# Performance work log

Measured on AMD Instinct MI355X. Metric: run time of the kernel, lower is better.

Reference implementation:

```python
import jax, jax.numpy as jnp
import numpy as np

NUM_GRAPHS = 512
NODES_PER_GRAPH = 128
HIDDEN = 64
K = 24


def _param(key, shape, scale=0.05):
    return jax.random.normal(key, shape, dtype=jnp.float32) * scale


def setup_inputs() -> dict:
    key = jax.random.key(0)
    ks = jax.random.split(key, 24)
    N = NUM_GRAPHS * NODES_PER_GRAPH
    inp = {
        "x_pf": jax.random.normal(ks[0], (N, 4), dtype=jnp.float32),
        "batch_pf": jnp.repeat(jnp.arange(NUM_GRAPHS, dtype=jnp.int64), NODES_PER_GRAPH),
        # pf_encode: Linear(4,64), ELU, Linear(64,64), ELU
        "we1": _param(ks[1], (4, HIDDEN)), "be1": _param(ks[2], (HIDDEN,)),
        "we2": _param(ks[3], (HIDDEN, HIDDEN)), "be2": _param(ks[4], (HIDDEN,)),
        # three DynamicEdgeConv edge MLPs: Linear(128,64)+ELU
        "wc1": _param(ks[5], (2 * HIDDEN, HIDDEN)), "bc1": _param(ks[6], (HIDDEN,)),
        "wc2": _param(ks[7], (2 * HIDDEN, HIDDEN)), "bc2": _param(ks[8], (HIDDEN,)),
        "wc3": _param(ks[9], (2 * HIDDEN, HIDDEN)), "bc3": _param(ks[10], (HIDDEN,)),
        # output MLP 64->64->32->32->8->1
        "wo1": _param(ks[11], (HIDDEN, 64)), "bo1": _param(ks[12], (64,)),
        "wo2": _param(ks[13], (64, 32)), "bo2": _param(ks[14], (32,)),
        "wo3": _param(ks[15], (32, 32)), "bo3": _param(ks[16], (32,)),
        "wo4": _param(ks[17], (32, 8)), "bo4": _param(ks[18], (8,)),
        "wo5": _param(ks[19], (8, 1)), "bo5": _param(ks[20], (1,)),
    }
    return inp


def dynamic_edge_conv(x, wc, bc):
    """x: [G,P,D]. kNN (incl. self) in feature space per graph, edge feature
    [x_i, x_j - x_i] -> Linear+ELU -> max over neighbors. Matches PyG
    DynamicEdgeConv(nn, k, aggr='max')."""
    sq = jnp.sum(x * x, axis=-1)                                   # [G,P]
    d = sq[:, :, None] + sq[:, None, :] - 2.0 * jnp.einsum('gpd,gqd->gpq', x, x)
    _, idx = jax.lax.top_k(-d, K)                                   # [G,P,K] nearest (self included, dist 0)
    xj = jax.vmap(lambda xg, ig: xg[ig])(x, idx)                    # [G,P,K,D]
    xi = x[:, :, None, :]
    e = jnp.concatenate([jnp.broadcast_to(xi, xj.shape), xj - xi], axis=-1)  # [G,P,K,2D]
    h = jax.nn.elu(e @ wc + bc)                                     # [G,P,K,D]
    return jnp.max(h, axis=2)                                       # [G,P,D]


def reference(x_pf, batch_pf, we1, be1, we2, be2, wc1, bc1, wc2, bc2, wc3, bc3,
              wo1, bo1, wo2, bo2, wo3, bo3, wo4, bo4, wo5, bo5):
    elu = jax.nn.elu
    h = elu(elu(x_pf @ we1 + be1) @ we2 + be2)                      # [N,64]
    h = h.reshape(NUM_GRAPHS, NODES_PER_GRAPH, HIDDEN)              # equal-size graphs
    h = dynamic_edge_conv(h, wc1, bc1)
    h = dynamic_edge_conv(h, wc2, bc2)
    h = dynamic_edge_conv(h, wc3, bc3)
    pooled = jnp.sum(h, axis=1)                                     # global_add_pool -> [G,64]
    o = elu(pooled @ wo1 + bo1)
    o = elu(o @ wo2 + bo2)
    o = elu(o @ wo3 + bo3)
    o = elu(o @ wo4 + bo4)
    out = o @ wo5 + bo5                                             # [G,1]
    return (out, batch_pf)
```

## Files before the change

kernel.cpp:

```cpp
#include <hip/hip_runtime.h>
#include <math.h>

#define NG 512
#define NP 128
#define HID 64
#define KNN 24
#define NTOT (NG*NP)

typedef __attribute__((ext_vector_type(8)))  short  short8;
typedef __attribute__((ext_vector_type(16))) float  floatx16;

__device__ __forceinline__ float elu_f(float v) { return v > 0.0f ? v : expm1f(v); }

__device__ __forceinline__ void split_bf16(float x, unsigned short& hb, unsigned short& lb) {
    unsigned u = __float_as_uint(x);
    unsigned h = (u + 0x7FFFu + ((u >> 16) & 1u)) >> 16;
    hb = (unsigned short)h;
    float hf = __uint_as_float(h << 16);
    float lo = x - hf;
    unsigned v = __float_as_uint(lo);
    lb = (unsigned short)((v + 0x7FFFu + ((v >> 16) & 1u)) >> 16);
}
__device__ __forceinline__ unsigned short bf_rne(float x) {
    unsigned u = __float_as_uint(x);
    return (unsigned short)((u + 0x7FFFu + ((u >> 16) & 1u)) >> 16);
}
__device__ __forceinline__ float bf_lo(unsigned u) { return __uint_as_float(u << 16); }
__device__ __forceinline__ float bf_hi(unsigned u) { return __uint_as_float(u & 0xFFFF0000u); }

__device__ __forceinline__ unsigned short* hchunk(unsigned short* base, int row, int ch) {
    return base + (((row << 4) + (ch ^ (row & 15))) << 3);
}
__device__ __forceinline__ const unsigned short* hchunk(const unsigned short* base, int row, int ch) {
    return base + (((row << 4) + (ch ^ (row & 15))) << 3);
}

__device__ __forceinline__ void sort8_asc(unsigned* y) {
    #pragma unroll
    for (int k = 2; k <= 8; k <<= 1)
        #pragma unroll
        for (int j = k >> 1; j > 0; j >>= 1)
            #pragma unroll
            for (int i = 0; i < 8; ++i) {
                const int l = i ^ j;
                if (l > i) {
                    const bool up = ((i & k) == 0);
                    const unsigned a = y[i], b = y[l];
                    const unsigned mn = a < b ? a : b;
                    const unsigned mx = a < b ? b : a;
                    y[i] = up ? mn : mx;
                    y[l] = up ? mx : mn;
                }
            }
}

__device__ __forceinline__ void merge_top24(unsigned* x) {
    #pragma unroll
    for (int d = 16; d > 0; d >>= 1)
        #pragma unroll
        for (int i = 0; i < 32; ++i)
            if (!(i & d) && i < 24) {
                const int l = i | d;
                const unsigned a = x[i], b = x[l];
                x[i] = a < b ? a : b;
                x[l] = a < b ? b : a;
            }
}

__global__ __launch_bounds__(256) void pack_w(
    const float* __restrict__ wc1, const float* __restrict__ wc2, const float* __restrict__ wc3,
    const float* __restrict__ we2,
    unsigned short* __restrict__ wp)
{
    const int n = blockIdx.x*256 + threadIdx.x;
    if (n < 24576) {
        const int layer = n >> 13;
        const int r = n & 8191;
        const int e = r & 7, j = (r >> 3) & 127, ch = r >> 10;
        const int k = (ch >> 1)*16 + (ch & 1)*8 + e;
        const float* wc = (layer == 0) ? wc1 : ((layer == 1) ? wc2 : wc3);
        float w;
        if (j < 64) w = wc[k*64 + j] - wc[(k+64)*64 + j];
        else        w = wc[(k+64)*64 + (j-64)];
        unsigned short hb, lb;
        split_bf16(w, hb, lb);
        unsigned short* base = wp + layer*16384;
        base[r] = hb;
        base[8192 + r] = lb;
    } else if (n < 24576 + 4096) {
        const int m = n - 24576;
        const int e = m & 7, col = (m >> 3) & 63, ch = m >> 9;
        const int k = (ch >> 1)*16 + (ch & 1)*8 + e;
        unsigned short hb, lb;
        split_bf16(we2[k*64 + col], hb, lb);
        unsigned short* base = wp + 49152;
        base[m] = hb;
        base[4096 + m] = lb;
    }
}

__global__ __launch_bounds__(512, 4) void conv_all(
    const float* __restrict__ x,
    const unsigned short* __restrict__ wp,
    const float* __restrict__ bc1, const float* __restrict__ bc2, const float* __restrict__ bc3,
    const float* __restrict__ we1, const float* __restrict__ be1,
    const unsigned short* __restrict__ we2p, const float* __restrict__ be2,
    float* __restrict__ ag_all, float* __restrict__ pooled_out, float* __restrict__ out_batch)
{
    __shared__ __align__(16) char arena[54784];
    unsigned*        keys  = (unsigned*)arena;
    unsigned*        nnidx = (unsigned*)(arena + 18432);
    unsigned short*  hilo  = (unsigned short*)(arena + 21504);
    float*           sqs   = (float*)(arena + 54272);

    const int g = blockIdx.x;
    const int t = threadIdx.x;
    const int w = t >> 6, lane = t & 63;
    const int lj = lane & 31, half = lane >> 5;
    const int rt = w & 3, wg = w >> 2;
    const int i2 = t & 127, s4 = t >> 7;
    float* __restrict__ ag = ag_all + (size_t)g * (NP*HID);

    {
        float* w1s = (float*)arena;
        float* b1v = (float*)(arena + 1024);
        float* b2v = (float*)(arena + 1280);
        if (t < 256) w1s[t] = we1[t];
        else if (t < 320) b1v[t-256] = be1[t-256];
        else if (t < 384) b2v[t-320] = be2[t-320];
        if (t < 128) out_batch[(size_t)g*128 + t] = (float)g;
        __syncthreads();

        const int n = t & 127, fh = t >> 7, f0 = fh*16;
        const float4 xv = ((const float4*)x)[g*128 + n];
        float acc1[16];
        #pragma unroll
        for (int q = 0; q < 4; ++q) {
            const float4 b4 = *(const float4*)(b1v + f0 + q*4);
            acc1[q*4+0] = b4.x; acc1[q*4+1] = b4.y; acc1[q*4+2] = b4.z; acc1[q*4+3] = b4.w;
        }
        #pragma unroll
        for (int k = 0; k < 4; ++k) {
            const float xk_ = (k == 0) ? xv.x : (k == 1) ? xv.y : (k == 2) ? xv.z : xv.w;
            #pragma unroll
            for (int q = 0; q < 4; ++q) {
                const float4 w4 = *(const float4*)(w1s + k*64 + f0 + q*4);
                acc1[q*4+0] = fmaf(xk_, w4.x, acc1[q*4+0]);
                acc1[q*4+1] = fmaf(xk_, w4.y, acc1[q*4+1]);
                acc1[q*4+2] = fmaf(xk_, w4.z, acc1[q*4+2]);
                acc1[q*4+3] = fmaf(xk_, w4.w, acc1[q*4+3]);
            }
        }
        unsigned hu[8], lu[8];
        #pragma unroll
        for (int e = 0; e < 8; ++e) {
            const float v0 = elu_f(acc1[2*e]), v1 = elu_f(acc1[2*e+1]);
            unsigned short h0, l0, h1, l1;
            split_bf16(v0, h0, l0); split_bf16(v1, h1, l1);
            hu[e] = (unsigned)h0 | ((unsigned)h1 << 16);
            lu[e] = (unsigned)l0 | ((unsigned)l1 << 16);
        }
        *(uint4*)hchunk(hilo, n, fh*2)       = make_uint4(hu[0], hu[1], hu[2], hu[3]);
        *(uint4*)hchunk(hilo, n, fh*2 + 1)   = make_uint4(hu[4], hu[5], hu[6], hu[7]);
        *(uint4*)hchunk(hilo, n, 8 + fh*2)   = make_uint4(lu[0], lu[1], lu[2], lu[3]);
        *(uint4*)hchunk(hilo, n, 8 + fh*2+1) = make_uint4(lu[4], lu[5], lu[6], lu[7]);
        __syncthreads();

        const int jt2 = wg;
        floatx16 acc = {0.f,0.f,0.f,0.f,0.f,0.f,0.f,0.f,0.f,0.f,0.f,0.f,0.f,0.f,0.f,0.f};
        #pragma unroll
        for (int p = 0; p < 3; ++p) {
            const int aSel = (p == 2) ? 8 : 0;
            const int part = (p == 1) ? 1 : 0;
            short8 af[4], bf4[4];
            #pragma unroll
            for (int c = 0; c < 4; ++c) {
                af[c]  = *(const short8*)hchunk(hilo, rt*32 + lj, aSel + c*2 + half);
                bf4[c] = *(const short8*)((const short*)we2p + part*4096 + (((c*2 + half)*64) + jt2*32 + lj)*8);
            }
            #pragma unroll
            for (int c = 0; c < 4; ++c) acc = __builtin_amdgcn_mfma_f32_32x32x16_bf16(af[c], bf4[c], acc, 0, 0, 0);
        }
        const int col = jt2*32 + lj;
        const float bias = b2v[col];
        __syncthreads();
        #pragma unroll
        for (int reg = 0; reg < 16; ++reg) {
            const int row = (reg & 3) + 8*(reg >> 2) + 4*half + rt*32;
            const float v = elu_f(acc[reg] + bias);
            unsigned short hb, lb;
            split_bf16(v, hb, lb);
            *(hchunk(hilo, row, col >> 3) + (col & 7))       = hb;
            *(hchunk(hilo, row, 8 + (col >> 3)) + (col & 7)) = lb;
        }
        __syncthreads();

        const int r = t >> 2, cq = t & 3, c0 = cq*2;
        const uint4 h0 = *(const uint4*)hchunk(hilo, r, c0);
        const uint4 h1 = *(const uint4*)hchunk(hilo, r, c0+1);
        const uint4 l0 = *(const uint4*)hchunk(hilo, r, 8+c0);
        const uint4 l1 = *(const uint4*)hchunk(hilo, r, 8+c0+1);
        float s = 0.0f;
        const unsigned hh[8] = {h0.x,h0.y,h0.z,h0.w,h1.x,h1.y,h1.z,h1.w};
        const unsigned ll[8] = {l0.x,l0.y,l0.z,l0.w,l1.x,l1.y,l1.z,l1.w};
        #pragma unroll
        for (int e = 0; e < 8; ++e) {
            const float va = bf_lo(hh[e]) + bf_lo(ll[e]);
            const float vb = bf_hi(hh[e]) + bf_hi(ll[e]);
            s = fmaf(va, va, s); s = fmaf(vb, vb, s);
        }
        s += __shfl_xor(s, 1);
        s += __shfl_xor(s, 2);
        if (cq == 0) sqs[r] = s;
        __syncthreads();
    }

    #pragma unroll 1
    for (int L = 0; L < 3; ++L) {
        const unsigned short* wpl = wp + L*16384;
        const float* bcl = (L == 0) ? bc1 : (L == 1) ? bc2 : bc3;

        unsigned xk[32];
        #pragma unroll
        for (int s = 0; s < 24; ++s) xk[s] = 0xFFFFFFFFu;

        #pragma unroll 1
        for (int jt = 0; jt < 4; ++jt) {
            if (wg == (jt & 1)) {
                floatx16 acc = {0.f,0.f,0.f,0.f,0.f,0.f,0.f,0.f,0.f,0.f,0.f,0.f,0.f,0.f,0.f,0.f};
                #pragma unroll
                for (int p = 0; p < 3; ++p) {
                    const int aSel = (p == 2) ? 8 : 0;
                    const int bSel = (p == 1) ? 8 : 0;
                    short8 af[4], bf4[4];
                    #pragma unroll
                    for (int c = 0; c < 4; ++c) {
                        af[c]  = *(const short8*)hchunk(hilo, rt*32 + lj, aSel + c*2 + half);
                        bf4[c] = *(const short8*)hchunk(hilo, jt*32 + lj, bSel + c*2 + half);
                    }
                    #pragma unroll
                    for (int c = 0; c < 4; ++c) acc = __builtin_amdgcn_mfma_f32_32x32x16_bf16(af[c], bf4[c], acc, 0, 0, 0);
                }
                const unsigned jg = (unsigned)(jt*32 + lj);
                const float sqj = sqs[jg];
                #pragma unroll
                for (int reg = 0; reg < 16; ++reg) {
                    const int i = (reg & 3) + 8*(reg >> 2) + 4*half + rt*32;
                    float d = fmaf(-2.0f, acc[reg], sqs[i] + sqj);
                    d = fmaxf(d, 0.0f);
                    keys[i*36 + lj] = (__float_as_uint(d) & 0xFFFFFF80u) | jg;
                }
            }
            __syncthreads();
            {
                const unsigned* kr = keys + i2*36 + s4*8;
                const uint4 k0 = *(const uint4*)kr;
                const uint4 k1 = *(const uint4*)(kr + 4);
                unsigned y[8] = {k0.x, k0.y, k0.z, k0.w, k1.x, k1.y, k1.z, k1.w};
                sort8_asc(y);
                #pragma unroll
                for (int e = 0; e < 8; ++e) xk[24+e] = y[7-e];
                merge_top24(xk);
            }
            __syncthreads();
        }

        #pragma unroll 1
        for (int src = 1; src < 4; ++src) {
            if (s4 == src) {
                #pragma unroll
                for (int e = 0; e < 24; ++e) keys[i2*36 + 12 + e] = xk[e];
            }
            __syncthreads();
            if (s4 == 0) {
                #pragma unroll 1
                for (int b = 0; b < 3; ++b) {
                    #pragma unroll
                    for (int e = 0; e < 8; ++e) xk[24+e] = keys[i2*36 + 12 + b*8 + (7-e)];
                    merge_top24(xk);
                }
            }
            __syncthreads();
        }
        if (s4 == 0) {
            #pragma unroll
            for (int c = 0; c < 6; ++c)
                nnidx[i2*6 + c] = (xk[c*4] & 127u) | ((xk[c*4+1] & 127u) << 8)
                                | ((xk[c*4+2] & 127u) << 16) | ((xk[c*4+3] & 127u) << 24);
        }
        __syncthreads();

        unsigned short* bs = (unsigned short*)arena;
        {
            short8 afr[8];
            #pragma unroll
            for (int sel = 0; sel < 2; ++sel)
                #pragma unroll
                for (int c = 0; c < 4; ++c)
                    afr[sel*4+c] = *(const short8*)hchunk(hilo, rt*32 + lj, sel*8 + c*2 + half);

            #pragma unroll 1
            for (int q2 = 0; q2 < 2; ++q2) {
                const int jt = wg*2 + q2;
                short8 bfr[8];
                #pragma unroll
                for (int part = 0; part < 2; ++part)
                    #pragma unroll
                    for (int c = 0; c < 4; ++c)
                        bfr[part*4+c] = *(const short8*)((const short*)wpl + part*8192 + (((c*2 + half)*128) + jt*32 + lj)*8);
                floatx16 acc = {0.f,0.f,0.f,0.f,0.f,0.f,0.f,0.f,0.f,0.f,0.f,0.f,0.f,0.f,0.f,0.f};
                #pragma unroll
                for (int c = 0; c < 4; ++c) acc = __builtin_amdgcn_mfma_f32_32x32x16_bf16(afr[c],   bfr[c],   acc, 0, 0, 0);
                #pragma unroll
                for (int c = 0; c < 4; ++c) acc = __builtin_amdgcn_mfma_f32_32x32x16_bf16(afr[c],   bfr[4+c], acc, 0, 0, 0);
                #pragma unroll
                for (int c = 0; c < 4; ++c) acc = __builtin_amdgcn_mfma_f32_32x32x16_bf16(afr[4+c], bfr[c],   acc, 0, 0, 0);

                if (wg == 0) {
                    const int col = jt*32 + lj;
                    const float bias = bcl[col];
                    #pragma unroll
                    for (int reg = 0; reg < 16; ++reg) {
                        const int row = (reg & 3) + 8*(reg >> 2) + 4*half + rt*32;
                        ag[(size_t)row*64 + col] = acc[reg] + bias;
                    }
                } else {
                    const int colb = q2*32 + lj;
                    #pragma unroll
                    for (int reg = 0; reg < 16; ++reg) {
                        const int row = (reg & 3) + 8*(reg >> 2) + 4*half + rt*32;
                        bs[row*68 + colb] = bf_rne(acc[reg]);
                    }
                }
            }
        }
        __syncthreads();

        {
            const int q = lane >> 4, fq = lane & 15;
            float4 psum = make_float4(0.f, 0.f, 0.f, 0.f);
            #pragma unroll 1
            for (int rg = 0; rg < 4; ++rg) {
                const int row = w*16 + rg*4 + q;
                float4 m = make_float4(-3e38f, -3e38f, -3e38f, -3e38f);
                #pragma unroll
                for (int c = 0; c < 6; ++c) {
                    const unsigned pk = nnidx[row*6 + c];
                    #pragma unroll
                    for (int e = 0; e < 4; ++e) {
                        const int j = (pk >> (8*e)) & 127;
                        const uint2 bb = *(const uint2*)(bs + j*68 + fq*4);
                        m.x = fmaxf(m.x, bf_lo(bb.x)); m.y = fmaxf(m.y, bf_hi(bb.x));
                        m.z = fmaxf(m.z, bf_lo(bb.y)); m.w = fmaxf(m.w, bf_hi(bb.y));
                    }
                }
                const float4 av = *(const float4*)(ag + (size_t)row*64 + fq*4);
                float4 o;
                o.x = elu_f(av.x + m.x); o.y = elu_f(av.y + m.y);
                o.z = elu_f(av.z + m.z); o.w = elu_f(av.w + m.w);

                if (L < 2) {
                    unsigned short hx,lx,hy,ly,hz,lz,hw2,lw2;
                    split_bf16(o.x,hx,lx); split_bf16(o.y,hy,ly);
                    split_bf16(o.z,hz,lz); split_bf16(o.w,hw2,lw2);
                    *(uint2*)(hchunk(hilo, row, fq >> 1) + (fq & 1)*4) =
                        make_uint2((unsigned)hx | ((unsigned)hy << 16), (unsigned)hz | ((unsigned)hw2 << 16));
                    *(uint2*)(hchunk(hilo, row, 8 + (fq >> 1)) + (fq & 1)*4) =
                        make_uint2((unsigned)lx | ((unsigned)ly << 16), (unsigned)lz | ((unsigned)lw2 << 16));
                    float sp = o.x*o.x + o.y*o.y + o.z*o.z + o.w*o.w;
                    sp += __shfl_xor(sp, 1);
                    sp += __shfl_xor(sp, 2);
                    sp += __shfl_xor(sp, 4);
                    sp += __shfl_xor(sp, 8);
                    if (fq == 0) sqs[row] = sp;
                } else {
                    psum.x += o.x; psum.y += o.y; psum.z += o.z; psum.w += o.w;
                }
            }
            if (L < 2) {
                __syncthreads();
            } else {
                __syncthreads();
                float* pool8 = (float*)(arena + 18432);
                psum.x += __shfl_xor(psum.x, 16); psum.y += __shfl_xor(psum.y, 16);
                psum.z += __shfl_xor(psum.z, 16); psum.w += __shfl_xor(psum.w, 16);
                psum.x += __shfl_xor(psum.x, 32); psum.y += __shfl_xor(psum.y, 32);
                psum.z += __shfl_xor(psum.z, 32); psum.w += __shfl_xor(psum.w, 32);
                if (q == 0) *(float4*)(pool8 + w*64 + fq*4) = psum;
                __syncthreads();
                if (t < 64) {
                    float s = 0.0f;
                    #pragma unroll
                    for (int k = 0; k < 8; ++k) s += pool8[k*64 + t];
                    pooled_out[(size_t)g*64 + t] = s;
                }
            }
        }
    }
}

__global__ __launch_bounds__(64) void head_kernel(
    const float* __restrict__ pooled_in,
    const float* __restrict__ wo1, const float* __restrict__ bo1,
    const float* __restrict__ wo2, const float* __restrict__ bo2,
    const float* __restrict__ wo3, const float* __restrict__ bo3,
    const float* __restrict__ wo4, const float* __restrict__ bo4,
    const float* __restrict__ wo5, const float* __restrict__ bo5,
    float* __restrict__ outp)
{
    __shared__ float pooled[64];
    __shared__ float o1[64];
    __shared__ float o2[32];
    __shared__ float o3[32];
    __shared__ float o4[8];
    const int g = blockIdx.x, t = threadIdx.x;

    pooled[t] = pooled_in[(size_t)g*64 + t];
    {
        float acc = bo1[t];
        #pragma unroll
        for (int k = 0; k < 64; ++k) acc = fmaf(pooled[k], wo1[k*64 + t], acc);
        o1[t] = elu_f(acc);
    }
    if (t < 32) {
        float acc = bo2[t];
        #pragma unroll
        for (int k = 0; k < 64; ++k) acc = fmaf(o1[k], wo2[k*32 + t], acc);
        o2[t] = elu_f(acc);
    }
    if (t < 32) {
        float acc = bo3[t];
        #pragma unroll
        for (int k = 0; k < 32; ++k) acc = fmaf(o2[k], wo3[k*32 + t], acc);
        o3[t] = elu_f(acc);
    }
    if (t < 8) {
        float acc = bo4[t];
        #pragma unroll
        for (int k = 0; k < 32; ++k) acc = fmaf(o3[k], wo4[k*8 + t], acc);
        o4[t] = elu_f(acc);
    }
    if (t == 0) {
        float acc = bo5[0];
        #pragma unroll
        for (int k = 0; k < 8; ++k) acc = fmaf(o4[k], wo5[k], acc);
        outp[g] = acc;
    }
}

extern "C" void kernel_launch(void* const* d_in, const int* in_sizes, int n_in,
                              void* d_out, int out_size, void* d_ws, size_t ws_size,
                              hipStream_t stream) {
    const float* x_pf = (const float*)d_in[0];
    const float* we1 = (const float*)d_in[2];
    const float* be1 = (const float*)d_in[3];
    const float* we2 = (const float*)d_in[4];
    const float* be2 = (const float*)d_in[5];
    const float* wc1 = (const float*)d_in[6];
    const float* bc1 = (const float*)d_in[7];
    const float* wc2 = (const float*)d_in[8];
    const float* bc2 = (const float*)d_in[9];
    const float* wc3 = (const float*)d_in[10];
    const float* bc3 = (const float*)d_in[11];
    const float* wo1 = (const float*)d_in[12];
    const float* bo1 = (const float*)d_in[13];
    const float* wo2 = (const float*)d_in[14];
    const float* bo2 = (const float*)d_in[15];
    const float* wo3 = (const float*)d_in[16];
    const float* bo3 = (const float*)d_in[17];
    const float* wo4 = (const float*)d_in[18];
    const float* bo4 = (const float*)d_in[19];
    const float* wo5 = (const float*)d_in[20];
    const float* bo5 = (const float*)d_in[21];

    float* out = (float*)d_out;
    char* ws = (char*)d_ws;
    float* abuf   = (float*)(ws);
    float* pooled = (float*)(ws + (size_t)16*1024*1024);
    unsigned short* wpack = (unsigned short*)(ws + (size_t)17*1024*1024);

    pack_w<<<112, 256, 0, stream>>>(wc1, wc2, wc3, we2, wpack);

    conv_all<<<NG, 512, 0, stream>>>(x_pf, wpack, bc1, bc2, bc3,
        we1, be1, wpack + 49152, be2, abuf, pooled, out + NG);

    head_kernel<<<NG, 64, 0, stream>>>(pooled, wo1, bo1, wo2, bo2, wo3, bo3, wo4, bo4, wo5, bo5, out);
}
```

Baseline: 188.9 us.

## Keep per-node linear term in LDS and use packed u16 max for aggregation

The per-node 'a' term (x_i part of the edge linear layer) now stays in shared memory, overlaying the hilo buffer, instead of going through a global workspace. This removes global writes and reads per layer, at the cost of an extra barrier and of deferring the hilo writeback into a separate pass with register-held outputs. Neighbour messages are stored as order-preserving 16-bit keys so the max over neighbours uses v_pk_max_u16 on two lanes at once. The key row stride shrinks from 36 to 33 to make room in LDS, which also changes the bank mapping.

```diff
diff --git a/kernel.cpp b/kernel.cpp
--- a/kernel.cpp
+++ b/kernel.cpp
@@ -27,6 +27,19 @@
 }
 __device__ __forceinline__ float bf_lo(unsigned u) { return __uint_as_float(u << 16); }
 __device__ __forceinline__ float bf_hi(unsigned u) { return __uint_as_float(u & 0xFFFF0000u); }
+
+__device__ __forceinline__ unsigned short f_to_key(unsigned short b) {
+    return (unsigned short)(b ^ ((b & 0x8000u) ? 0xFFFFu : 0x8000u));
+}
+__device__ __forceinline__ float key_to_f(unsigned k) {
+    const unsigned bf = (k & 0x8000u) ? (k ^ 0x8000u) : (k ^ 0xFFFFu);
+    return __uint_as_float(bf << 16);
+}
+__device__ __forceinline__ unsigned pk_max_u16(unsigned a, unsigned b) {
+    unsigned d;
+    asm("v_pk_max_u16 %0, %1, %2" : "=v"(d) : "v"(a), "v"(b));
+    return d;
+}
 
 __device__ __forceinline__ unsigned short* hchunk(unsigned short* base, int row, int ch) {
     return base + (((row << 4) + (ch ^ (row & 15))) << 3);
@@ -105,13 +118,13 @@
     const float* __restrict__ bc1, const float* __restrict__ bc2, const float* __restrict__ bc3,
     const float* __restrict__ we1, const float* __restrict__ be1,
     const unsigned short* __restrict__ we2p, const float* __restrict__ be2,
-    float* __restrict__ ag_all, float* __restrict__ pooled_out, float* __restrict__ out_batch)
+    float* __restrict__ pooled_out, float* __restrict__ out_batch)
 {
-    __shared__ __align__(16) char arena[54784];
+    __shared__ __align__(16) char arena[53760];
     unsigned*        keys  = (unsigned*)arena;
-    unsigned*        nnidx = (unsigned*)(arena + 18432);
-    unsigned short*  hilo  = (unsigned short*)(arena + 21504);
-    float*           sqs   = (float*)(arena + 54272);
+    unsigned*        nnidx = (unsigned*)(arena + 17408);
+    unsigned short*  hilo  = (unsigned short*)(arena + 20480);
+    float*           sqs   = (float*)(arena + 53248);
 
     const int g = blockIdx.x;
     const int t = threadIdx.x;
@@ -119,7 +132,6 @@
     const int lj = lane & 31, half = lane >> 5;
     const int rt = w & 3, wg = w >> 2;
     const int i2 = t & 127, s4 = t >> 7;
-    float* __restrict__ ag = ag_all + (size_t)g * (NP*HID);
 
     {
         float* w1s = (float*)arena;
@@ -248,12 +260,12 @@
                     const int i = (reg & 3) + 8*(reg >> 2) + 4*half + rt*32;
                     float d = fmaf(-2.0f, acc[reg], sqs[i] + sqj);
                     d = fmaxf(d, 0.0f);
-                    keys[i*36 + lj] = (__float_as_uint(d) & 0xFFFFFF80u) | jg;
+                    keys[i*33 + lj] = (__float_as_uint(d) & 0xFFFFFF80u) | jg;
                 }
             }
             __syncthreads();
             {
-                const unsigned* kr = keys + i2*36 + s4*8;
+                const unsigned* kr = keys + i2*33 + s4*8;
                 const uint4 k0 = *(const uint4*)kr;
                 const uint4 k1 = *(const uint4*)(kr + 4);
                 unsigned y[8] = {k0.x, k0.y, k0.z, k0.w, k1.x, k1.y, k1.z, k1.w};
@@ -269,14 +281,14 @@
         for (int src = 1; src < 4; ++src) {
             if (s4 == src) {
                 #pragma unroll
-                for (int e = 0; e < 24; ++e) keys[i2*36 + 12 + e] = xk[e];
+                for (int e = 0; e < 24; ++e) keys[i2*33 + 9 + e] = xk[e];
             }
             __syncthreads();
             if (s4 == 0) {
                 #pragma unroll 1
                 for (int b = 0; b < 3; ++b) {
                     #pragma unroll
-                    for (int e = 0; e < 8; ++e) xk[24+e] = keys[i2*36 + 12 + b*8 + (7-e)];
+                    for (int e = 0; e < 8; ++e) xk[24+e] = keys[i2*33 + 9 + b*8 + (7-e)];
                     merge_top24(xk);
                 }
             }
@@ -291,6 +303,7 @@
         __syncthreads();
 
         unsigned short* bs = (unsigned short*)arena;
+        float* af32 = (float*)(arena + 20480);
         {
             short8 afr[8];
             #pragma unroll
@@ -298,6 +311,7 @@
                 #pragma unroll
                 for (int c = 0; c < 4; ++c)
                     afr[sel*4+c] = *(const short8*)hchunk(hilo, rt*32 + lj, sel*8 + c*2 + half);
+            __syncthreads();
 
             #pragma unroll 1
             for (int q2 = 0; q2 < 2; ++q2) {
@@ -322,14 +336,14 @@
                     #pragma unroll
                     for (int reg = 0; reg < 16; ++reg) {
                         const int row = (reg & 3) + 8*(reg >> 2) + 4*half + rt*32;
-                        ag[(size_t)row*64 + col] = acc[reg] + bias;
+                        af32[row*64 + col] = acc[reg] + bias;
                     }
                 } else {
                     const int colb = q2*32 + lj;
                     #pragma unroll
                     for (int reg = 0; reg < 16; ++reg) {
                         const int row = (reg & 3) + 8*(reg >> 2) + 4*half + rt*32;
-                        bs[row*68 + colb] = bf_rne(acc[reg]);
+                        bs[row*68 + colb] = f_to_key(bf_rne(acc[reg]));
                     }
                 }
             }
@@ -339,10 +353,11 @@
         {
             const int q = lane >> 4, fq = lane & 15;
             float4 psum = make_float4(0.f, 0.f, 0.f, 0.f);
-            #pragma unroll 1
+            float4 osave[4];
+            #pragma unroll
             for (int rg = 0; rg < 4; ++rg) {
                 const int row = w*16 + rg*4 + q;
-                float4 m = make_float4(-3e38f, -3e38f, -3e38f, -3e38f);
+                unsigned mk0 = 0u, mk1 = 0u;
                 #pragma unroll
                 for (int c = 0; c < 6; ++c) {
                     const unsigned pk = nnidx[row*6 + c];
@@ -350,23 +365,19 @@
                     for (int e = 0; e < 4; ++e) {
                         const int j = (pk >> (8*e)) & 127;
                         const uint2 bb = *(const uint2*)(bs + j*68 + fq*4);
-                        m.x = fmaxf(m.x, bf_lo(bb.x)); m.y = fmaxf(m.y, bf_hi(bb.x));
-                        m.z = fmaxf(m.z, bf_lo(bb.y)); m.w = fmaxf(m.w, bf_hi(bb.y));
+                        mk0 = pk_max_u16(mk0, bb.x);
+                        mk1 = pk_max_u16(mk1, bb.y);
                     }
                 }
-                const float4 av = *(const float4*)(ag + (size_t)row*64 + fq*4);
+                const float4 av = *(const float4*)(af32 + row*64 + fq*4);
                 float4 o;
-                o.x = elu_f(av.x + m.x); o.y = elu_f(av.y + m.y);
-                o.z = elu_f(av.z + m.z); o.w = elu_f(av.w + m.w);
+                o.x = elu_f(av.x + key_to_f(mk0 & 0xFFFFu));
+                o.y = elu_f(av.y + key_to_f(mk0 >> 16));
+                o.z = elu_f(av.z + key_to_f(mk1 & 0xFFFFu));
+                o.w = elu_f(av.w + key_to_f(mk1 >> 16));
 
                 if (L < 2) {
-                    unsigned short hx,lx,hy,ly,hz,lz,hw2,lw2;
-                    split_bf16(o.x,hx,lx); split_bf16(o.y,hy,ly);
-                    split_bf16(o.z,hz,lz); split_bf16(o.w,hw2,lw2);
-                    *(uint2*)(hchunk(hilo, row, fq >> 1) + (fq & 1)*4) =
-                        make_uint2((unsigned)hx | ((unsigned)hy << 16), (unsigned)hz | ((unsigned)hw2 << 16));
-                    *(uint2*)(hchunk(hilo, row, 8 + (fq >> 1)) + (fq & 1)*4) =
-                        make_uint2((unsigned)lx | ((unsigned)ly << 16), (unsigned)lz | ((unsigned)lw2 << 16));
+                    osave[rg] = o;
                     float sp = o.x*o.x + o.y*o.y + o.z*o.z + o.w*o.w;
                     sp += __shfl_xor(sp, 1);
                     sp += __shfl_xor(sp, 2);
@@ -379,9 +390,22 @@
             }
             if (L < 2) {
                 __syncthreads();
+                #pragma unroll
+                for (int rg = 0; rg < 4; ++rg) {
+                    const int row = w*16 + rg*4 + q;
+                    const float4 o = osave[rg];
+                    unsigned short hx,lx,hy,ly,hz,lz,hw2,lw2;
+                    split_bf16(o.x,hx,lx); split_bf16(o.y,hy,ly);
+                    split_bf16(o.z,hz,lz); split_bf16(o.w,hw2,lw2);
+                    *(uint2*)(hchunk(hilo, row, fq >> 1) + (fq & 1)*4) =
+                        make_uint2((unsigned)hx | ((unsigned)hy << 16), (unsigned)hz | ((unsigned)hw2 << 16));
+                    *(uint2*)(hchunk(hilo, row, 8 + (fq >> 1)) + (fq & 1)*4) =
+                        make_uint2((unsigned)lx | ((unsigned)ly << 16), (unsigned)lz | ((unsigned)lw2 << 16));
+                }
+                __syncthreads();
             } else {
                 __syncthreads();
-                float* pool8 = (float*)(arena + 18432);
+                float* pool8 = (float*)(arena + 17408);
                 psum.x += __shfl_xor(psum.x, 16); psum.y += __shfl_xor(psum.y, 16);
                 psum.z += __shfl_xor(psum.z, 16); psum.w += __shfl_xor(psum.w, 16);
                 psum.x += __shfl_xor(psum.x, 32); psum.y += __shfl_xor(psum.y, 32);
@@ -475,14 +499,13 @@
 
     float* out = (float*)d_out;
     char* ws = (char*)d_ws;
-    float* abuf   = (float*)(ws);
-    float* pooled = (float*)(ws + (size_t)16*1024*1024);
-    unsigned short* wpack = (unsigned short*)(ws + (size_t)17*1024*1024);
+    unsigned short* wpack = (unsigned short*)ws;
+    float* pooled = (float*)(ws + 131072);
 
     pack_w<<<112, 256, 0, stream>>>(wc1, wc2, wc3, we2, wpack);
 
     conv_all<<<NG, 512, 0, stream>>>(x_pf, wpack, bc1, bc2, bc3,
-        we1, be1, wpack + 49152, be2, abuf, pooled, out + NG);
+        we1, be1, wpack + 49152, be2, pooled, out + NG);
 
     head_kernel<<<NG, 64, 0, stream>>>(pooled, wo1, bo1, wo2, bo2, wo3, bo3, wo4, bo4, wo5, bo5, out);
 }
```

Result: slower. 195.5 us (+3.5%).
